# Performance work log

Measured on AMD Instinct MI355X. Metric: run time of the kernel, lower is better.

## Reference

```python
import jax, jax.numpy as jnp
import numpy as np

BS, T, HS, WS = 2, 4, 32, 32
HW = HS * WS
D, NH, NL, NP = 256, 8, 4, 4
HD = D // NH
DFFN = 1024


def layer_norm(x, g, b, eps=1e-5):
    mu = jnp.mean(x, axis=-1, keepdims=True)
    var = jnp.mean((x - mu) ** 2, axis=-1, keepdims=True)
    return (x - mu) * jax.lax.rsqrt(var + eps) * g + b


def bilinear_gather(val, loc, Hl, Wl):
    # val: (bs, nh, Hl*Wl, hd); loc: (bs, Lq, nh, P, 2) in [0,1], last dim (x, y)
    # matches F.grid_sample(align_corners=False, padding_mode='zeros') on grid=2*loc-1
    x = loc[..., 0] * Wl - 0.5
    y = loc[..., 1] * Hl - 0.5
    x0 = jnp.floor(x)
    y0 = jnp.floor(y)
    lx = x - x0
    ly = y - y0
    bs, Lq, nh, P = x.shape
    out = jnp.zeros((bs, nh, Lq * P, val.shape[-1]), val.dtype)
    for dy in (0, 1):
        for dx in (0, 1):
            xi = x0 + dx
            yi = y0 + dy
            w = (lx if dx else 1.0 - lx) * (ly if dy else 1.0 - ly)
            valid = (xi >= 0) & (xi < Wl) & (yi >= 0) & (yi < Hl)
            w = jnp.where(valid, w, 0.0)
            xi_c = jnp.clip(xi, 0, Wl - 1).astype(jnp.int32)
            yi_c = jnp.clip(yi, 0, Hl - 1).astype(jnp.int32)
            idx = (yi_c * Wl + xi_c).transpose(0, 2, 1, 3).reshape(bs, nh, Lq * P)
            g = jnp.take_along_axis(val, idx[..., None], axis=2)
            wt = w.transpose(0, 2, 1, 3).reshape(bs, nh, Lq * P)
            out = out + wt[..., None] * g
    return out.reshape(bs, nh, Lq, P, val.shape[-1])


def setup_inputs() -> dict:
    key = jax.random.key(0)
    ks = jax.random.split(key, 12)
    s = 0.02
    return {
        "src": jax.random.normal(ks[0], (BS, T, HW, D), jnp.float32),
        "pos": jax.random.normal(ks[1], (BS, T, HW, D), jnp.float32),
        "reference_points": jax.random.uniform(ks[2], (BS, T * HW, NL, 2), jnp.float32),
        "value_proj_w": jax.random.normal(ks[3], (D, D), jnp.float32) * s,
        "value_proj_b": jnp.zeros((D,), jnp.float32),
        "sampling_offsets_w": jax.random.normal(ks[4], (D, NH * NL * NP * 2), jnp.float32) * s,
        "sampling_offsets_b": jax.random.normal(ks[5], (NH * NL * NP * 2,), jnp.float32) * s,
        "attn_weights_w": jax.random.normal(ks[6], (D, NH * NL * NP), jnp.float32) * s,
        "attn_weights_b": jnp.zeros((NH * NL * NP,), jnp.float32),
        "output_proj_w": jax.random.normal(ks[7], (D, D), jnp.float32) * s,
        "output_proj_b": jnp.zeros((D,), jnp.float32),
        "norm1_g": jnp.ones((D,), jnp.float32),
        "norm1_b": jnp.zeros((D,), jnp.float32),
        "linear1_w": jax.random.normal(ks[8], (D, DFFN), jnp.float32) * s,
        "linear1_b": jnp.zeros((DFFN,), jnp.float32),
        "linear2_w": jax.random.normal(ks[9], (DFFN, D), jnp.float32) * s,
        "linear2_b": jnp.zeros((D,), jnp.float32),
        "norm2_g": jnp.ones((D,), jnp.float32),
        "norm2_b": jnp.zeros((D,), jnp.float32),
        "spatial_shapes": np.array([[HS, WS]] * NL, np.int32),
        "level_start_index": np.arange(NL, dtype=np.int32) * HW,
    }


def reference(src, pos, reference_points, value_proj_w, value_proj_b,
              sampling_offsets_w, sampling_offsets_b, attn_weights_w, attn_weights_b,
              output_proj_w, output_proj_b, norm1_g, norm1_b,
              linear1_w, linear1_b, linear2_w, linear2_b, norm2_g, norm2_b,
              spatial_shapes, level_start_index):
    bs, t, hw, d = src.shape
    Lq = t * hw
    x = src.reshape(bs, Lq, d)
    q = x  # module never adds pos in forward (with_pos_embed unused)
    value = (x @ value_proj_w + value_proj_b).reshape(bs, Lq, NH, HD)
    offsets = (q @ sampling_offsets_w + sampling_offsets_b).reshape(bs, Lq, NH, NL, NP, 2)
    aw = jax.nn.softmax((q @ attn_weights_w + attn_weights_b).reshape(bs, Lq, NH, NL * NP), axis=-1)
    aw = aw.reshape(bs, Lq, NH, NL, NP)
    ss = np.asarray(spatial_shapes)
    lsi = np.asarray(level_start_index)
    offset_normalizer = jnp.asarray(ss[:, ::-1].copy(), src.dtype)  # (L, 2) = (W, H)
    sampling_locations = reference_points[:, :, None, :, None, :] + offsets / offset_normalizer[None, None, None, :, None, :]
    attn_out = jnp.zeros((bs, NH, Lq, HD), src.dtype)
    for l in range(NL):
        Hl, Wl = int(ss[l, 0]), int(ss[l, 1])
        start = int(lsi[l])
        v_l = value[:, start:start + Hl * Wl].transpose(0, 2, 1, 3)  # (bs, nh, HlWl, hd)
        samp = bilinear_gather(v_l, sampling_locations[:, :, :, l], Hl, Wl)  # (bs, nh, Lq, P, hd)
        w_l = aw[:, :, :, l].transpose(0, 2, 1, 3)  # (bs, nh, Lq, P)
        attn_out = attn_out + jnp.sum(samp * w_l[..., None], axis=3)
    attn_out = attn_out.transpose(0, 2, 1, 3).reshape(bs, Lq, d) @ output_proj_w + output_proj_b
    x = layer_norm(x + attn_out, norm1_g, norm1_b)
    ffn = jax.nn.relu(x @ linear1_w + linear1_b) @ linear2_w + linear2_b
    x = layer_norm(x + ffn, norm2_g, norm2_b)
    return x.reshape(bs, t, hw, d), sampling_locations
```

## Files before the change

kernel.cpp:

```cpp
#include <hip/hip_runtime.h>
#include <math.h>

#define ROWS   8192
#define LQ     4096
#define NHEAD  8
#define NLVL   4
#define NPTS   4
#define HDIM   32

typedef __attribute__((ext_vector_type(8))) short v8s;
typedef __attribute__((ext_vector_type(4))) float v4f;
typedef __attribute__((ext_vector_type(8))) unsigned short v8u;

__device__ __forceinline__ unsigned short f2bf(float x) {
    unsigned int u = __float_as_uint(x);
    u += 0x7fffu + ((u >> 16) & 1u);
    return (unsigned short)(u >> 16);
}
__device__ __forceinline__ float bf2f(unsigned short x) {
    return __uint_as_float(((unsigned int)x) << 16);
}

__device__ __forceinline__ void glds16(const void* g, void* l) {
    __builtin_amdgcn_global_load_lds(
        (const __attribute__((address_space(1))) unsigned int*)g,
        (__attribute__((address_space(3))) unsigned int*)l, 16, 0, 0);
}

__device__ __forceinline__ void trans_tile(const float* __restrict__ in,
                                           unsigned short* __restrict__ out,
                                           int K, int N, int ldout, int n_off,
                                           int bx, int by, int tid)
{
    __shared__ float t[32][33];
    int tx = tid & 31, ty = tid >> 5;
    int k0 = by << 5, n0 = bx << 5;
    #pragma unroll
    for (int i = 0; i < 4; i++)
        t[ty + i * 8][tx] = in[(size_t)(k0 + ty + i * 8) * N + n0 + tx];
    __syncthreads();
    #pragma unroll
    for (int i = 0; i < 4; i++)
        out[(size_t)(n_off + n0 + ty + i * 8) * ldout + k0 + tx] = f2bf(t[tx][ty + i * 8]);
}

__global__ __launch_bounds__(256) void prep_k(
    const float* __restrict__ vw, const float* __restrict__ ofw,
    const float* __restrict__ aww, const float* __restrict__ pw,
    const float* __restrict__ w1, const float* __restrict__ w2,
    unsigned short* __restrict__ Btcat, unsigned short* __restrict__ pwT,
    unsigned short* __restrict__ w1T, unsigned short* __restrict__ w2T,
    const float* __restrict__ vb, const float* __restrict__ ofb,
    const float* __restrict__ awb, float* __restrict__ biascat)
{
    int bid = blockIdx.x, tid = threadIdx.x;
    if (bid < 64) {
        int t = bid; trans_tile(vw, Btcat, 256, 256, 256, 0, t & 7, t >> 3, tid);
    } else if (bid < 128) {
        int t = bid - 64; trans_tile(ofw, Btcat, 256, 256, 256, 256, t & 7, t >> 3, tid);
    } else if (bid < 160) {
        int t = bid - 128; trans_tile(aww, Btcat, 256, 128, 256, 512, t & 3, t >> 2, tid);
    } else if (bid < 224) {
        int t = bid - 160; trans_tile(pw, pwT, 256, 256, 256, 0, t & 7, t >> 3, tid);
    } else if (bid < 480) {
        int t = bid - 224; trans_tile(w1, w1T, 256, 1024, 256, 0, t & 31, t >> 5, tid);
    } else if (bid < 736) {
        int t = bid - 480; trans_tile(w2, w2T, 1024, 256, 1024, 0, t & 7, t >> 3, tid);
    } else {
        biascat[tid] = vb[tid];
        biascat[tid + 256] = ofb[tid];
        if (tid < 128) biascat[tid + 512] = awb[tid];
    }
}

template<bool PROJ, bool AF32, bool OUTBF, bool RELU, bool RES>
__global__ __launch_bounds__(256) void mfma_gemm128_k(
    const void* __restrict__ Araw,
    const unsigned short* __restrict__ Bt,
    const float* __restrict__ bias,
    const float* __restrict__ res,
    void* __restrict__ Cout,
    unsigned short* __restrict__ vbf,
    const float* __restrict__ refp,
    float* __restrict__ oloc,
    int M, int N, int K)
{
    __shared__ __align__(16) unsigned short As[2048];
    __shared__ __align__(16) unsigned short Bs[4096];
    const int tid = threadIdx.x;
    const int row0 = blockIdx.y << 6, col0 = blockIdx.x << 7;
    const int wid = tid >> 6, lane = tid & 63;
    const int wm = wid & 1, wn = wid >> 1;
    const int lr = lane & 15, kq = lane >> 4;

    v4f acc[2][4];
    #pragma unroll
    for (int i = 0; i < 2; i++)
        #pragma unroll
        for (int j = 0; j < 4; j++) acc[i][j] = (v4f){0.f, 0.f, 0.f, 0.f};

    for (int k0 = 0; k0 < K; k0 += 32) {
        float4 af0, af1;
        if constexpr (AF32) {
            const float* Af = (const float*)Araw;
            int r1 = tid >> 2, kk1 = ((tid & 3) + (r1 >> 2)) & 3;
            const float* p1 = Af + (size_t)(row0 + r1) * K + k0 + kk1 * 8;
            af0 = *(const float4*)p1; af1 = *(const float4*)(p1 + 4);
        }
        __syncthreads();
        if constexpr (AF32) {
            v8u u1;
            u1[0] = f2bf(af0.x); u1[1] = f2bf(af0.y); u1[2] = f2bf(af0.z); u1[3] = f2bf(af0.w);
            u1[4] = f2bf(af1.x); u1[5] = f2bf(af1.y); u1[6] = f2bf(af1.z); u1[7] = f2bf(af1.w);
            *(v8u*)(&As[tid * 8]) = u1;
        } else {
            const unsigned short* A = (const unsigned short*)Araw;
            int c = wid * 64 + lane;
            int row = c >> 2;
            int kk = ((c & 3) + (row >> 2)) & 3;
            glds16(A + (size_t)(row0 + row) * K + k0 + kk * 8,
                   &As[(wid * 64) * 8]);
        }
        #pragma unroll
        for (int i = 0; i < 2; i++) {
            int c = wid * 128 + i * 64 + lane;
            int row = c >> 2;
            int kk = ((c & 3) + (row >> 2)) & 3;
            glds16(Bt + (size_t)(col0 + row) * K + k0 + kk * 8,
                   &Bs[(wid * 128 + i * 64) * 8]);
        }
        __syncthreads();
        v8s bf[4];
        #pragma unroll
        for (int nt = 0; nt < 4; nt++) {
            int row = wn * 64 + nt * 16 + lr;
            int s = (kq - (row >> 2)) & 3;
            bf[nt] = *(const v8s*)(&Bs[(row * 4 + s) * 8]);
        }
        #pragma unroll
        for (int mt = 0; mt < 2; mt++) {
            int row = wm * 32 + mt * 16 + lr;
            int s = (kq - (row >> 2)) & 3;
            v8s af = *(const v8s*)(&As[(row * 4 + s) * 8]);
            #pragma unroll
            for (int nt = 0; nt < 4; nt++)
                acc[mt][nt] = __builtin_amdgcn_mfma_f32_16x16x32_bf16(af, bf[nt], acc[mt][nt], 0, 0, 0);
        }
    }

    const int rq = lane >> 4;
    #pragma unroll
    for (int mt = 0; mt < 2; mt++) {
        #pragma unroll
        for (int nt = 0; nt < 4; nt++) {
            int col = col0 + wn * 64 + nt * 16 + lr;
            float bv = bias[col];
            #pragma unroll
            for (int i = 0; i < 4; i++) {
                int row = row0 + wm * 32 + mt * 16 + rq * 4 + i;
                float v = acc[mt][nt][i] + bv;
                if (RELU) v = fmaxf(v, 0.f);
                if (RES)  v += res[(size_t)row * N + col];
                if (PROJ) {
                    if (col < 256) {
                        int b = row >> 12, rb = row & 4095;
                        int l = rb >> 10, pix = rb & 1023;
                        int h = col >> 5, d = col & 31;
                        size_t idx = ((size_t)(((b << 2) + l) * 8 + h) << 15) + (pix << 5) + d;
                        vbf[idx] = f2bf(v);
                    } else if (col < 512) {
                        int colm = col - 256;
                        int l = (colm >> 3) & 3, cc = colm & 1;
                        oloc[(size_t)row * 256 + colm] =
                            refp[(size_t)row * 8 + l * 2 + cc] + v * (1.f / 32.f);
                    } else {
                        ((float*)Cout)[(size_t)row * 128 + col - 512] = v;
                    }
                } else if (OUTBF) {
                    ((unsigned short*)Cout)[(size_t)row * N + col] = f2bf(v);
                } else {
                    ((float*)Cout)[(size_t)row * N + col] = v;
                }
            }
        }
    }
}

template<bool OUTBF, bool RELU, bool RESBF>
__global__ __launch_bounds__(256) void mfma_gemm64_k(
    const unsigned short* __restrict__ A,
    const unsigned short* __restrict__ Bt,
    const float* __restrict__ bias,
    const unsigned short* __restrict__ resbf,
    void* __restrict__ Cout,
    int M, int N, int K)
{
    __shared__ __align__(16) unsigned short As[2048];
    __shared__ __align__(16) unsigned short Bs[2048];
    const int tid = threadIdx.x;
    const int row0 = blockIdx.y << 6, col0 = blockIdx.x << 6;
    const int wid = tid >> 6, lane = tid & 63;
    const int lr = lane & 15, kq = lane >> 4;

    v4f acc[4];
    #pragma unroll
    for (int i = 0; i < 4; i++) acc[i] = (v4f){0.f, 0.f, 0.f, 0.f};

    for (int k0 = 0; k0 < K; k0 += 32) {
        __syncthreads();
        {
            int c = wid * 64 + lane;
            int row = c >> 2;
            int kk = ((c & 3) + (row >> 2)) & 3;
            glds16(A + (size_t)(row0 + row) * K + k0 + kk * 8, &As[wid * 512]);
            glds16(Bt + (size_t)(col0 + row) * K + k0 + kk * 8, &Bs[wid * 512]);
        }
        __syncthreads();
        int colr = wid * 16 + lr;
        int sb = (kq - (colr >> 2)) & 3;
        v8s bf = *(const v8s*)(&Bs[(colr * 4 + sb) * 8]);
        #pragma unroll
        for (int mt = 0; mt < 4; mt++) {
            int rowr = mt * 16 + lr;
            int sa = (kq - (rowr >> 2)) & 3;
            v8s af = *(const v8s*)(&As[(rowr * 4 + sa) * 8]);
            acc[mt] = __builtin_amdgcn_mfma_f32_16x16x32_bf16(af, bf, acc[mt], 0, 0, 0);
        }
    }

    const int rq = lane >> 4;
    const int col = col0 + wid * 16 + lr;
    float bv = bias[col];
    #pragma unroll
    for (int mt = 0; mt < 4; mt++) {
        #pragma unroll
        for (int i = 0; i < 4; i++) {
            int row = row0 + mt * 16 + rq * 4 + i;
            float v = acc[mt][i] + bv;
            if (RELU) v = fmaxf(v, 0.f);
            if (RESBF) v += bf2f(resbf[(size_t)row * N + col]);
            if (OUTBF) ((unsigned short*)Cout)[(size_t)row * N + col] = f2bf(v);
            else       ((float*)Cout)[(size_t)row * N + col] = v;
        }
    }
}

__global__ __launch_bounds__(256) void mfma_gemm_ln_k(
    const unsigned short* __restrict__ A,
    const unsigned short* __restrict__ Bt,
    const float* __restrict__ bias,
    const float* __restrict__ res,
    const float* __restrict__ g,
    const float* __restrict__ b,
    unsigned short* __restrict__ outbf,
    int M, int K)
{
    __shared__ __align__(16) unsigned short As[1024];
    __shared__ __align__(16) unsigned short Bs[8192];
    __shared__ float red[2][32][4];
    const int tid = threadIdx.x;
    const int row0 = blockIdx.x << 5;
    const int wid = tid >> 6, lane = tid & 63;
    const int lr = lane & 15, kq = lane >> 4;
    const int rq = kq;

    v4f acc[2][4];
    #pragma unroll
    for (int i = 0; i < 2; i++)
        #pragma unroll
        for (int j = 0; j < 4; j++) acc[i][j] = (v4f){0.f, 0.f, 0.f, 0.f};

    for (int k0 = 0; k0 < K; k0 += 32) {
        __syncthreads();
        if (wid < 2) {
            int c = wid * 64 + lane;
            int row = c >> 2;
            int kk = ((c & 3) + (row >> 2)) & 3;
            glds16(A + (size_t)(row0 + row) * K + k0 + kk * 8,
                   &As[(wid * 64) * 8]);
        }
        #pragma unroll
        for (int i = 0; i < 4; i++) {
            int c = (wid * 4 + i) * 64 + lane;
            int col = c >> 2;
            int kk = ((c & 3) + (col >> 2)) & 3;
            glds16(Bt + (size_t)col * K + k0 + kk * 8,
                   &Bs[((wid * 4 + i) * 64) * 8]);
        }
        __syncthreads();
        v8s bf[4];
        #pragma unroll
        for (int ct = 0; ct < 4; ct++) {
            int col = wid * 64 + ct * 16 + lr;
            int s = (kq - (col >> 2)) & 3;
            bf[ct] = *(const v8s*)(&Bs[(col * 4 + s) * 8]);
        }
        #pragma unroll
        for (int rt = 0; rt < 2; rt++) {
            int rowl = rt * 16 + lr;
            int s = (kq - (rowl >> 2)) & 3;
            v8s af = *(const v8s*)(&As[(rowl * 4 + s) * 8]);
            #pragma unroll
            for (int ct = 0; ct < 4; ct++)
                acc[rt][ct] = __builtin_amdgcn_mfma_f32_16x16x32_bf16(af, bf[ct], acc[rt][ct], 0, 0, 0);
        }
    }

    float t[2][4][4];
    float s1[2][4], s2[2][4];
    #pragma unroll
    for (int rt = 0; rt < 2; rt++)
        #pragma unroll
        for (int i = 0; i < 4; i++) { s1[rt][i] = 0.f; s2[rt][i] = 0.f; }
    #pragma unroll
    for (int rt = 0; rt < 2; rt++) {
        #pragma unroll
        for (int ct = 0; ct < 4; ct++) {
            int col = wid * 64 + ct * 16 + lr;
            float bv = bias[col];
            #pragma unroll
            for (int i = 0; i < 4; i++) {
                int row = row0 + rt * 16 + rq * 4 + i;
                float v = acc[rt][ct][i] + bv + res[(size_t)row * 256 + col];
                t[rt][ct][i] = v;
                s1[rt][i] += v;
                s2[rt][i] += v * v;
            }
        }
    }
    #pragma unroll
    for (int o = 1; o < 16; o <<= 1) {
        #pragma unroll
        for (int rt = 0; rt < 2; rt++)
            #pragma unroll
            for (int i = 0; i < 4; i++) {
                s1[rt][i] += __shfl_xor(s1[rt][i], o);
                s2[rt][i] += __shfl_xor(s2[rt][i], o);
            }
    }
    if (lr == 0) {
        #pragma unroll
        for (int rt = 0; rt < 2; rt++)
            #pragma unroll
            for (int i = 0; i < 4; i++) {
                int rl = rt * 16 + rq * 4 + i;
                red[0][rl][wid] = s1[rt][i];
                red[1][rl][wid] = s2[rt][i];
            }
    }
    __syncthreads();
    float mu[2][4], rstd[2][4];
    #pragma unroll
    for (int rt = 0; rt < 2; rt++) {
        #pragma unroll
        for (int i = 0; i < 4; i++) {
            int rl = rt * 16 + rq * 4 + i;
            float S1 = red[0][rl][0] + red[0][rl][1] + red[0][rl][2] + red[0][rl][3];
            float S2 = red[1][rl][0] + red[1][rl][1] + red[1][rl][2] + red[1][rl][3];
            float m = S1 * (1.f / 256.f);
            mu[rt][i] = m;
            rstd[rt][i] = rsqrtf(S2 * (1.f / 256.f) - m * m + 1e-5f);
        }
    }
    #pragma unroll
    for (int rt = 0; rt < 2; rt++) {
        #pragma unroll
        for (int ct = 0; ct < 4; ct++) {
            int col = wid * 64 + ct * 16 + lr;
            float gg = g[col], bb = b[col];
            #pragma unroll
            for (int i = 0; i < 4; i++) {
                int row = row0 + rt * 16 + rq * 4 + i;
                float o = (t[rt][ct][i] - mu[rt][i]) * rstd[rt][i] * gg + bb;
                outbf[(size_t)row * 256 + col] = f2bf(o);
            }
        }
    }
}

__global__ __launch_bounds__(256) void fused_gather_k(
    const float* __restrict__ po,
    const unsigned short* __restrict__ vbf,
    const float* __restrict__ loc,
    unsigned short* __restrict__ attn_bf)
{
    int tid = threadIdx.x;
    int g = tid >> 4, l = (tid >> 2) & 3, d8 = tid & 3;
    int h = blockIdx.x & 7;
    int r = (blockIdx.x >> 3) * 16 + g;
    int b = r >> 12;

    float locv[8];
    *(float4*)(locv)     = *(const float4*)(loc + (size_t)r * 256 + h * 32 + l * 8);
    *(float4*)(locv + 4) = *(const float4*)(loc + (size_t)r * 256 + h * 32 + l * 8 + 4);

    float w4[4];
    *(float4*)(w4) = *(const float4*)(po + (size_t)r * 128 + h * 16 + l * 4);
    float m = fmaxf(fmaxf(w4[0], w4[1]), fmaxf(w4[2], w4[3]));
    m = fmaxf(m, __shfl_xor(m, 4));
    m = fmaxf(m, __shfl_xor(m, 8));
    float s = 0.f;
    #pragma unroll
    for (int p = 0; p < 4; p++) { w4[p] = __expf(w4[p] - m); s += w4[p]; }
    s += __shfl_xor(s, 4);
    s += __shfl_xor(s, 8);
    float inv = 1.f / s;

    const unsigned short* vbase =
        vbf + (((size_t)(((b << 2) + l) * 8 + h)) << 15) + d8 * 8;

    float acc[8];
    #pragma unroll
    for (int k = 0; k < 8; k++) acc[k] = 0.f;

    #pragma unroll
    for (int pp = 0; pp < 2; pp++) {
        v8u uv[8];
        float cw[8];
        #pragma unroll
        for (int p2 = 0; p2 < 2; p2++) {
            int p = pp * 2 + p2;
            float xf = locv[p * 2] * 32.f - 0.5f, yf = locv[p * 2 + 1] * 32.f - 0.5f;
            float x0f = floorf(xf), y0f = floorf(yf);
            float fx = xf - x0f, fy = yf - y0f;
            int x0 = (int)x0f, y0 = (int)y0f;
            float wgt = w4[p] * inv;
            #pragma unroll
            for (int dy = 0; dy < 2; dy++) {
                #pragma unroll
                for (int dx = 0; dx < 2; dx++) {
                    int idx = p2 * 4 + dy * 2 + dx;
                    int xi = x0 + dx, yi = y0 + dy;
                    float wt = (dx ? fx : 1.f - fx) * (dy ? fy : 1.f - fy);
                    bool valid = (xi >= 0) & (xi < 32) & (yi >= 0) & (yi < 32);
                    int xc = min(max(xi, 0), 31), yc = min(max(yi, 0), 31);
                    cw[idx] = valid ? (wgt * wt) : 0.f;
                    uv[idx] = *(const v8u*)(vbase + (size_t)((yc << 5) + xc) * 32);
                }
            }
        }
        #pragma unroll
        for (int idx = 0; idx < 8; idx++) {
            float c = cw[idx];
            #pragma unroll
            for (int k = 0; k < 8; k++)
                acc[k] += c * bf2f(uv[idx][k]);
        }
    }
    #pragma unroll
    for (int k = 0; k < 8; k++) {
        acc[k] += __shfl_xor(acc[k], 4);
        acc[k] += __shfl_xor(acc[k], 8);
    }
    if (l == 0) {
        v8u o;
        #pragma unroll
        for (int k = 0; k < 8; k++) o[k] = f2bf(acc[k]);
        *(v8u*)(attn_bf + (size_t)r * 256 + h * 32 + d8 * 8) = o;
    }
}

__global__ __launch_bounds__(256) void layernorm_k(
    float* __restrict__ x, const float* __restrict__ g, const float* __restrict__ b)
{
    int lane = threadIdx.x & 63;
    int wv = threadIdx.x >> 6;
    int row = blockIdx.x * 4 + wv;
    int c = lane << 2;
    float4 v = *(const float4*)(x + (size_t)row * 256 + c);
    float s = v.x + v.y + v.z + v.w;
    #pragma unroll
    for (int o = 1; o < 64; o <<= 1) s += __shfl_xor(s, o);
    float mu = s * (1.f / 256.f);
    float d0 = v.x - mu, d1 = v.y - mu, d2 = v.z - mu, d3 = v.w - mu;
    float vs = d0 * d0 + d1 * d1 + d2 * d2 + d3 * d3;
    #pragma unroll
    for (int o = 1; o < 64; o <<= 1) vs += __shfl_xor(vs, o);
    float rstd = rsqrtf(vs * (1.f / 256.f) + 1e-5f);
    float4 gg = *(const float4*)(g + c);
    float4 bb = *(const float4*)(b + c);
    float4 o4;
    o4.x = d0 * rstd * gg.x + bb.x;
    o4.y = d1 * rstd * gg.y + bb.y;
    o4.z = d2 * rstd * gg.z + bb.z;
    o4.w = d3 * rstd * gg.w + bb.w;
    *(float4*)(x + (size_t)row * 256 + c) = o4;
}

extern "C" void kernel_launch(void* const* d_in, const int* in_sizes, int n_in,
                              void* d_out, int out_size, void* d_ws, size_t ws_size,
                              hipStream_t stream)
{
    const float* src   = (const float*)d_in[0];
    const float* refp  = (const float*)d_in[2];
    const float* vw    = (const float*)d_in[3];
    const float* vb    = (const float*)d_in[4];
    const float* ofw   = (const float*)d_in[5];
    const float* ofb   = (const float*)d_in[6];
    const float* aww   = (const float*)d_in[7];
    const float* awb   = (const float*)d_in[8];
    const float* pw    = (const float*)d_in[9];
    const float* pb    = (const float*)d_in[10];
    const float* g1    = (const float*)d_in[11];
    const float* b1    = (const float*)d_in[12];
    const float* w1    = (const float*)d_in[13];
    const float* bi1   = (const float*)d_in[14];
    const float* w2    = (const float*)d_in[15];
    const float* bi2   = (const float*)d_in[16];
    const float* g2    = (const float*)d_in[17];
    const float* b2    = (const float*)d_in[18];

    float* ws = (float*)d_ws;
    float*          po        = ws;
    unsigned short* value_bf  = (unsigned short*)(ws + 1048576);
    unsigned short* x1_bf     = (unsigned short*)(ws + 2097152);
    unsigned short* attn_bf   = (unsigned short*)(ws + 3145728);
    unsigned short* hidden_bf = (unsigned short*)(ws + 4194304);
    unsigned short* Btcat     = (unsigned short*)(ws + 8388608);
    unsigned short* pwT       = (unsigned short*)(ws + 8470528);
    unsigned short* w1T       = (unsigned short*)(ws + 8503296);
    unsigned short* w2T       = (unsigned short*)(ws + 8634368);
    float*          biascat   = ws + 8765440;

    float* out_x   = (float*)d_out;
    float* out_loc = out_x + 2097152;

    dim3 blk(256);

    prep_k<<<737, blk, 0, stream>>>(vw, ofw, aww, pw, w1, w2,
                                    Btcat, pwT, w1T, w2T, vb, ofb, awb, biascat);

    mfma_gemm128_k<true, true, false, false, false><<<dim3(5, 128), blk, 0, stream>>>(
        src, Btcat, biascat, nullptr, po, value_bf, refp, out_loc, ROWS, 640, 256);

    fused_gather_k<<<4096, blk, 0, stream>>>(po, value_bf, out_loc, attn_bf);

    mfma_gemm_ln_k<<<256, blk, 0, stream>>>(
        attn_bf, pwT, pb, src, g1, b1, x1_bf, ROWS, 256);

    mfma_gemm128_k<false, false, true, true, false><<<dim3(8, 128), blk, 0, stream>>>(
        x1_bf, w1T, bi1, nullptr, hidden_bf, nullptr, nullptr, nullptr, ROWS, 1024, 256);

    mfma_gemm64_k<false, false, true><<<dim3(4, 128), blk, 0, stream>>>(
        hidden_bf, w2T, bi2, x1_bf, out_x, ROWS, 256, 1024);
    layernorm_k<<<2048, blk, 0, stream>>>(out_x, g2, b2);
}
```

Measured before the change: 181.1 us.

## Double-buffer LDS tiles in MFMA GEMMs and pre-convert src to bf16

Gives the three MFMA GEMM kernels two LDS buffers for A and B, so the async global-to-LDS load of the next K tile is issued before the current tile is computed, with one barrier per iteration instead of two. The fp32 src operand of the first projection GEMM is now converted to bf16 once, by extra blocks appended to the prep kernel. This lets that GEMM use the direct global-to-LDS load path instead of loading and converting fp32 in registers. In exchange, LDS per block doubles, which may reduce occupancy, and the extra src_bf buffer adds a write and a read of global memory.

```diff
diff --git a/kernel.cpp b/kernel.cpp
--- a/kernel.cpp
+++ b/kernel.cpp
@@ -51,7 +51,8 @@
     unsigned short* __restrict__ Btcat, unsigned short* __restrict__ pwT,
     unsigned short* __restrict__ w1T, unsigned short* __restrict__ w2T,
     const float* __restrict__ vb, const float* __restrict__ ofb,
-    const float* __restrict__ awb, float* __restrict__ biascat)
+    const float* __restrict__ awb, float* __restrict__ biascat,
+    const float* __restrict__ src, unsigned short* __restrict__ srcbf)
 {
     int bid = blockIdx.x, tid = threadIdx.x;
     if (bid < 64) {
@@ -66,60 +67,47 @@
         int t = bid - 224; trans_tile(w1, w1T, 256, 1024, 256, 0, t & 31, t >> 5, tid);
     } else if (bid < 736) {
         int t = bid - 480; trans_tile(w2, w2T, 1024, 256, 1024, 0, t & 7, t >> 3, tid);
-    } else {
+    } else if (bid == 736) {
         biascat[tid] = vb[tid];
         biascat[tid + 256] = ofb[tid];
         if (tid < 128) biascat[tid + 512] = awb[tid];
-    }
-}
-
-template<bool PROJ, bool AF32, bool OUTBF, bool RELU, bool RES>
+    } else {
+        int n = bid - 737;
+        size_t base = (size_t)n * 2048 + (size_t)tid * 8;
+        float4 a = *(const float4*)(src + base);
+        float4 b = *(const float4*)(src + base + 4);
+        v8u o;
+        o[0] = f2bf(a.x); o[1] = f2bf(a.y); o[2] = f2bf(a.z); o[3] = f2bf(a.w);
+        o[4] = f2bf(b.x); o[5] = f2bf(b.y); o[6] = f2bf(b.z); o[7] = f2bf(b.w);
+        *(v8u*)(srcbf + base) = o;
+    }
+}
+
+template<bool PROJ, bool OUTBF, bool RELU>
 __global__ __launch_bounds__(256) void mfma_gemm128_k(
-    const void* __restrict__ Araw,
+    const unsigned short* __restrict__ A,
     const unsigned short* __restrict__ Bt,
     const float* __restrict__ bias,
-    const float* __restrict__ res,
     void* __restrict__ Cout,
     unsigned short* __restrict__ vbf,
     const float* __restrict__ refp,
     float* __restrict__ oloc,
     int M, int N, int K)
 {
-    __shared__ __align__(16) unsigned short As[2048];
-    __shared__ __align__(16) unsigned short Bs[4096];
+    __shared__ __align__(16) unsigned short As[2][2048];
+    __shared__ __align__(16) unsigned short Bs[2][4096];
     const int tid = threadIdx.x;
     const int row0 = blockIdx.y << 6, col0 = blockIdx.x << 7;
     const int wid = tid >> 6, lane = tid & 63;
     const int wm = wid & 1, wn = wid >> 1;
     const int lr = lane & 15, kq = lane >> 4;
 
-    v4f acc[2][4];
-    #pragma unroll
-    for (int i = 0; i < 2; i++)
-        #pragma unroll
-        for (int j = 0; j < 4; j++) acc[i][j] = (v4f){0.f, 0.f, 0.f, 0.f};
-
-    for (int k0 = 0; k0 < K; k0 += 32) {
-        float4 af0, af1;
-        if constexpr (AF32) {
-            const float* Af = (const float*)Araw;
-            int r1 = tid >> 2, kk1 = ((tid & 3) + (r1 >> 2)) & 3;
-            const float* p1 = Af + (size_t)(row0 + r1) * K + k0 + kk1 * 8;
-            af0 = *(const float4*)p1; af1 = *(const float4*)(p1 + 4);
-        }
-        __syncthreads();
-        if constexpr (AF32) {
-            v8u u1;
-            u1[0] = f2bf(af0.x); u1[1] = f2bf(af0.y); u1[2] = f2bf(af0.z); u1[3] = f2bf(af0.w);
-            u1[4] = f2bf(af1.x); u1[5] = f2bf(af1.y); u1[6] = f2bf(af1.z); u1[7] = f2bf(af1.w);
-            *(v8u*)(&As[tid * 8]) = u1;
-        } else {
-            const unsigned short* A = (const unsigned short*)Araw;
-            int c = wid * 64 + lane;
+    auto stage = [&](int k0, int b) {
+        {
+            int c = tid;
             int row = c >> 2;
             int kk = ((c & 3) + (row >> 2)) & 3;
-            glds16(A + (size_t)(row0 + row) * K + k0 + kk * 8,
-                   &As[(wid * 64) * 8]);
+            glds16(A + (size_t)(row0 + row) * K + k0 + kk * 8, &As[b][(wid * 64) * 8]);
         }
         #pragma unroll
         for (int i = 0; i < 2; i++) {
@@ -127,25 +115,38 @@
             int row = c >> 2;
             int kk = ((c & 3) + (row >> 2)) & 3;
             glds16(Bt + (size_t)(col0 + row) * K + k0 + kk * 8,
-                   &Bs[(wid * 128 + i * 64) * 8]);
-        }
+                   &Bs[b][(wid * 128 + i * 64) * 8]);
+        }
+    };
+
+    v4f acc[2][4];
+    #pragma unroll
+    for (int i = 0; i < 2; i++)
+        #pragma unroll
+        for (int j = 0; j < 4; j++) acc[i][j] = (v4f){0.f, 0.f, 0.f, 0.f};
+
+    stage(0, 0);
+    int cur = 0;
+    for (int k0 = 0; k0 < K; k0 += 32) {
         __syncthreads();
+        if (k0 + 32 < K) stage(k0 + 32, cur ^ 1);
         v8s bf[4];
         #pragma unroll
         for (int nt = 0; nt < 4; nt++) {
             int row = wn * 64 + nt * 16 + lr;
             int s = (kq - (row >> 2)) & 3;
-            bf[nt] = *(const v8s*)(&Bs[(row * 4 + s) * 8]);
+            bf[nt] = *(const v8s*)(&Bs[cur][(row * 4 + s) * 8]);
         }
         #pragma unroll
         for (int mt = 0; mt < 2; mt++) {
             int row = wm * 32 + mt * 16 + lr;
             int s = (kq - (row >> 2)) & 3;
-            v8s af = *(const v8s*)(&As[(row * 4 + s) * 8]);
+            v8s af = *(const v8s*)(&As[cur][(row * 4 + s) * 8]);
             #pragma unroll
             for (int nt = 0; nt < 4; nt++)
                 acc[mt][nt] = __builtin_amdgcn_mfma_f32_16x16x32_bf16(af, bf[nt], acc[mt][nt], 0, 0, 0);
         }
+        cur ^= 1;
     }
 
     const int rq = lane >> 4;
@@ -160,7 +161,6 @@
                 int row = row0 + wm * 32 + mt * 16 + rq * 4 + i;
                 float v = acc[mt][nt][i] + bv;
                 if (RELU) v = fmaxf(v, 0.f);
-                if (RES)  v += res[(size_t)row * N + col];
                 if (PROJ) {
                     if (col < 256) {
                         int b = row >> 12, rb = row & 4095;
@@ -195,37 +195,41 @@
     void* __restrict__ Cout,
     int M, int N, int K)
 {
-    __shared__ __align__(16) unsigned short As[2048];
-    __shared__ __align__(16) unsigned short Bs[2048];
+    __shared__ __align__(16) unsigned short As[2][2048];
+    __shared__ __align__(16) unsigned short Bs[2][2048];
     const int tid = threadIdx.x;
     const int row0 = blockIdx.y << 6, col0 = blockIdx.x << 6;
     const int wid = tid >> 6, lane = tid & 63;
     const int lr = lane & 15, kq = lane >> 4;
 
+    auto stage = [&](int k0, int b) {
+        int c = tid;
+        int row = c >> 2;
+        int kk = ((c & 3) + (row >> 2)) & 3;
+        glds16(A + (size_t)(row0 + row) * K + k0 + kk * 8, &As[b][wid * 512]);
+        glds16(Bt + (size_t)(col0 + row) * K + k0 + kk * 8, &Bs[b][wid * 512]);
+    };
+
     v4f acc[4];
     #pragma unroll
     for (int i = 0; i < 4; i++) acc[i] = (v4f){0.f, 0.f, 0.f, 0.f};
 
+    stage(0, 0);
+    int cur = 0;
     for (int k0 = 0; k0 < K; k0 += 32) {
         __syncthreads();
-        {
-            int c = wid * 64 + lane;
-            int row = c >> 2;
-            int kk = ((c & 3) + (row >> 2)) & 3;
-            glds16(A + (size_t)(row0 + row) * K + k0 + kk * 8, &As[wid * 512]);
-            glds16(Bt + (size_t)(col0 + row) * K + k0 + kk * 8, &Bs[wid * 512]);
-        }
-        __syncthreads();
+        if (k0 + 32 < K) stage(k0 + 32, cur ^ 1);
         int colr = wid * 16 + lr;
         int sb = (kq - (colr >> 2)) & 3;
-        v8s bf = *(const v8s*)(&Bs[(colr * 4 + sb) * 8]);
+        v8s bf = *(const v8s*)(&Bs[cur][(colr * 4 + sb) * 8]);
         #pragma unroll
         for (int mt = 0; mt < 4; mt++) {
             int rowr = mt * 16 + lr;
             int sa = (kq - (rowr >> 2)) & 3;
-            v8s af = *(const v8s*)(&As[(rowr * 4 + sa) * 8]);
+            v8s af = *(const v8s*)(&As[cur][(rowr * 4 + sa) * 8]);
             acc[mt] = __builtin_amdgcn_mfma_f32_16x16x32_bf16(af, bf, acc[mt], 0, 0, 0);
         }
+        cur ^= 1;
     }
 
     const int rq = lane >> 4;
@@ -255,8 +259,8 @@
     unsigned short* __restrict__ outbf,
     int M, int K)
 {
-    __shared__ __align__(16) unsigned short As[1024];
-    __shared__ __align__(16) unsigned short Bs[8192];
+    __shared__ __align__(16) unsigned short As[2][1024];
+    __shared__ __align__(16) unsigned short Bs[2][8192];
     __shared__ float red[2][32][4];
     const int tid = threadIdx.x;
     const int row0 = blockIdx.x << 5;
@@ -264,46 +268,50 @@
     const int lr = lane & 15, kq = lane >> 4;
     const int rq = kq;
 
-    v4f acc[2][4];
-    #pragma unroll
-    for (int i = 0; i < 2; i++)
-        #pragma unroll
-        for (int j = 0; j < 4; j++) acc[i][j] = (v4f){0.f, 0.f, 0.f, 0.f};
-
-    for (int k0 = 0; k0 < K; k0 += 32) {
-        __syncthreads();
+    auto stage = [&](int k0, int bb) {
         if (wid < 2) {
             int c = wid * 64 + lane;
             int row = c >> 2;
             int kk = ((c & 3) + (row >> 2)) & 3;
-            glds16(A + (size_t)(row0 + row) * K + k0 + kk * 8,
-                   &As[(wid * 64) * 8]);
+            glds16(A + (size_t)(row0 + row) * K + k0 + kk * 8, &As[bb][(wid * 64) * 8]);
         }
         #pragma unroll
         for (int i = 0; i < 4; i++) {
             int c = (wid * 4 + i) * 64 + lane;
             int col = c >> 2;
             int kk = ((c & 3) + (col >> 2)) & 3;
-            glds16(Bt + (size_t)col * K + k0 + kk * 8,
-                   &Bs[((wid * 4 + i) * 64) * 8]);
-        }
+            glds16(Bt + (size_t)col * K + k0 + kk * 8, &Bs[bb][((wid * 4 + i) * 64) * 8]);
+        }
+    };
+
+    v4f acc[2][4];
+    #pragma unroll
+    for (int i = 0; i < 2; i++)
+        #pragma unroll
+        for (int j = 0; j < 4; j++) acc[i][j] = (v4f){0.f, 0.f, 0.f, 0.f};
+
+    stage(0, 0);
+    int cur = 0;
+    for (int k0 = 0; k0 < K; k0 += 32) {
         __syncthreads();
+        if (k0 + 32 < K) stage(k0 + 32, cur ^ 1);
         v8s bf[4];
         #pragma unroll
         for (int ct = 0; ct < 4; ct++) {
             int col = wid * 64 + ct * 16 + lr;
             int s = (kq - (col >> 2)) & 3;
-            bf[ct] = *(const v8s*)(&Bs[(col * 4 + s) * 8]);
+            bf[ct] = *(const v8s*)(&Bs[cur][(col * 4 + s) * 8]);
         }
         #pragma unroll
         for (int rt = 0; rt < 2; rt++) {
             int rowl = rt * 16 + lr;
             int s = (kq - (rowl >> 2)) & 3;
-            v8s af = *(const v8s*)(&As[(rowl * 4 + s) * 8]);
+            v8s af = *(const v8s*)(&As[cur][(rowl * 4 + s) * 8]);
             #pragma unroll
             for (int ct = 0; ct < 4; ct++)
                 acc[rt][ct] = __builtin_amdgcn_mfma_f32_16x16x32_bf16(af, bf[ct], acc[rt][ct], 0, 0, 0);
         }
+        cur ^= 1;
     }
 
     float t[2][4][4];
@@ -521,25 +529,27 @@
     unsigned short* w1T       = (unsigned short*)(ws + 8503296);
     unsigned short* w2T       = (unsigned short*)(ws + 8634368);
     float*          biascat   = ws + 8765440;
+    unsigned short* src_bf    = (unsigned short*)(ws + 8766080);
 
     float* out_x   = (float*)d_out;
     float* out_loc = out_x + 2097152;
 
     dim3 blk(256);
 
-    prep_k<<<737, blk, 0, stream>>>(vw, ofw, aww, pw, w1, w2,
-                                    Btcat, pwT, w1T, w2T, vb, ofb, awb, biascat);
-
-    mfma_gemm128_k<true, true, false, false, false><<<dim3(5, 128), blk, 0, stream>>>(
-        src, Btcat, biascat, nullptr, po, value_bf, refp, out_loc, ROWS, 640, 256);
+    prep_k<<<1761, blk, 0, stream>>>(vw, ofw, aww, pw, w1, w2,
+                                     Btcat, pwT, w1T, w2T, vb, ofb, awb, biascat,
+                                     src, src_bf);
+
+    mfma_gemm128_k<true, false, false><<<dim3(5, 128), blk, 0, stream>>>(
+        src_bf, Btcat, biascat, po, value_bf, refp, out_loc, ROWS, 640, 256);
 
     fused_gather_k<<<4096, blk, 0, stream>>>(po, value_bf, out_loc, attn_bf);
 
     mfma_gemm_ln_k<<<256, blk, 0, stream>>>(
         attn_bf, pwT, pb, src, g1, b1, x1_bf, ROWS, 256);
 
-    mfma_gemm128_k<false, false, true, true, false><<<dim3(8, 128), blk, 0, stream>>>(
-        x1_bf, w1T, bi1, nullptr, hidden_bf, nullptr, nullptr, nullptr, ROWS, 1024, 256);
+    mfma_gemm128_k<false, true, true><<<dim3(8, 128), blk, 0, stream>>>(
+        x1_bf, w1T, bi1, hidden_bf, nullptr, nullptr, nullptr, ROWS, 1024, 256);
 
     mfma_gemm64_k<false, false, true><<<dim3(4, 128), blk, 0, stream>>>(
         hidden_bf, w2T, bi2, x1_bf, out_x, ROWS, 256, 1024);
```

Result: no change. 181.5 us (+0.2%).
